# Optimization experiments

Hardware: AMD Instinct MI355X
Metric: run time of the kernel (lower is better)

The kernel has to match this reference:

```python
import jax, jax.numpy as jnp
import numpy as np

B, S1, S2, C = 8, 256, 256, 64
M1, M2 = 32, 32          # n_modes per spatial dim
SCALE = 1.0 / (C * C)    # 1/(in_channels*out_channels)


def setup_inputs() -> dict:
    key = jax.random.key(0)
    ks = jax.random.split(key, 5)
    X = jax.random.normal(ks[0], (B, S1, S2, C), dtype=jnp.float32)
    k0r = SCALE * jax.random.normal(ks[1], (M1, C, C), dtype=jnp.float32)
    k0i = SCALE * jax.random.normal(ks[2], (M1, C, C), dtype=jnp.float32)
    k1r = SCALE * jax.random.normal(ks[3], (M2, C, C), dtype=jnp.float32)
    k1i = SCALE * jax.random.normal(ks[4], (M2, C, C), dtype=jnp.float32)
    return {"X": X, "k0r": k0r, "k0i": k0i, "k1r": k1r, "k1i": k1i}


def reference(X, k0r, k0i, k1r, k1i):
    # Factorized spectral conv: per-spatial-dim rFFT -> truncated-mode
    # complex channel mix -> zero-pad -> irFFT, summed over dims.
    k0 = jax.lax.complex(k0r, k0i)  # (M1, out, in)
    k1 = jax.lax.complex(k1r, k1i)  # (M2, out, in)

    out = jnp.zeros_like(X)

    # --- spatial dim 0 (axis -3) ---
    Xf = jnp.fft.rfft(X, axis=-3, norm="forward")          # (B, S1//2+1, S2, C) complex
    Yt = jnp.einsum("rij,bryj->bryi", k0, Xf[:, :M1])       # truncated-mode channel mix
    Y = jnp.zeros_like(Xf).at[:, :M1].set(Yt)               # zero-pad back to full modes
    out = out + jnp.fft.irfft(Y, n=S1, axis=-3, norm="forward")

    # --- spatial dim 1 (axis -2) ---
    Xf = jnp.fft.rfft(X, axis=-2, norm="forward")           # (B, S1, S2//2+1, C)
    Yt = jnp.einsum("rij,bxrj->bxri", k1, Xf[:, :, :M2])
    Y = jnp.zeros_like(Xf).at[:, :, :M2].set(Yt)
    out = out + jnp.fft.irfft(Y, n=S2, axis=-2, norm="forward")

    return out
```

## Files before the change

### kernel.cpp

```cpp
#include <hip/hip_runtime.h>


namespace {

constexpr int S = 256, C = 64;

typedef _Float16 f16;
typedef _Float16 f16x2 __attribute__((ext_vector_type(2)));
typedef _Float16 f16x4 __attribute__((ext_vector_type(4)));
typedef _Float16 f16x8 __attribute__((ext_vector_type(8)));
typedef float f32x16 __attribute__((ext_vector_type(16)));
typedef unsigned int u32;

constexpr int OFF_FWDF = 0;
constexpr int OFF_INVF = 8192;
constexpr int OFF_A2   = 16384;
constexpr int OFF_PW   = 540672;
constexpr size_t WS_NEED = (size_t)OFF_PW * 4 + (size_t)8 * 256 * 256 * 64 * 2;

constexpr int P   = 4624;
constexpr int LDS_BYTES = 8 * P;

__device__ __host__ inline int cadr(int c) { return c * 16 + (c >> 3) * 16; }
__device__ inline int yadr(int r, int c) { return 1152 * r + c * 4 + (c >> 5) * 16; }

__global__ void k_init_all(const float* __restrict__ k0r, const float* __restrict__ k0i,
                           const float* __restrict__ k1r, const float* __restrict__ ki1,
                           float* __restrict__ ws) {
  const int bid = blockIdx.x;
  if (bid < 128) {
    int t = bid * 256 + threadIdx.x;
    f16* fwdF = (f16*)(ws + OFF_FWDF);
    f16* invF = (f16*)(ws + OFF_INVF);
    if (t < 16384) {
      int e = t & 7, lane = (t >> 3) & 63, mtkk = t >> 9;
      int mt = mtkk & 1, kk = mtkk >> 1;
      int mc = mt * 32 + (lane & 31);
      int x = kk * 16 + 8 * (lane >> 5) + e;
      int r = mc >> 1;
      float ang = (float)((r * x) & 255) * (3.14159265358979323846f / 128.0f);
      float v = (mc & 1) ? -sinf(ang) : cosf(ang);
      fwdF[t] = (f16)v;
    } else {
      int t2 = t - 16384;
      int e = t2 & 7, lane = (t2 >> 3) & 63, mtg = (t2 >> 9) & 7, kk = t2 >> 12;
      int u = mtg * 32 + (lane & 31);
      int mcv = kk * 16 + 8 * (lane >> 5) + e;
      int r = mcv >> 1;
      float wgt = (r == 0) ? 1.0f : 2.0f;
      float ang = (float)((r * u) & 255) * (3.14159265358979323846f / 128.0f);
      float v = (mcv & 1) ? -wgt * sinf(ang) : wgt * cosf(ang);
      invF[t2] = (f16)(v * (1.0f / 256.0f));
    }
    return;
  }
  const int db = bid - 128;
  const float* kr = (db < 2048) ? k0r : k1r;
  const float* ki = (db < 2048) ? k0i : ki1;
  f16* A2 = (f16*)(ws + OFF_A2) + ((db < 2048) ? 0 : 524288);
  int t = (db & 2047) * 256 + threadIdx.x;
  int e = t & 7, l = (t >> 3) & 63, kk = (t >> 9) & 7, mt = (t >> 12) & 3, r = t >> 14;
  int m = mt * 32 + (l & 31);
  int kreal = kk * 16 + 8 * (l >> 5) + e;
  int i = m >> 1, imo = m & 1, j = kreal >> 1, imi = kreal & 1;
  int src = (r * 64 + i) * 64 + j;
  float v = (imi == 0) ? ((imo == 0) ? kr[src] : ki[src])
                       : ((imo == 0) ? -ki[src] : kr[src]);
  A2[t] = (f16)v;
}

template <int MODE>
__launch_bounds__(512, 2)
__global__ void k_dim(const float* __restrict__ X, const float* __restrict__ ws,
                      float* __restrict__ out, f16* __restrict__ pw) {
  constexpr int DIM = (MODE == 0 || MODE == 2) ? 0 : 1;
  __shared__ char sm[LDS_BYTES] __attribute__((aligned(16)));

  const int tid = threadIdx.x;
  const int l = tid & 63, w = tid >> 6;
  const int g2 = l >> 5, l31 = l & 31;
  const int n0 = w * 32;
  const int bid = (DIM == 1) ? (int)(gridDim.x - 1 - blockIdx.x) : (int)blockIdx.x;
  const int b = bid >> 6;
  const int t4 = (bid & 63) * 4;
  const size_t bbase = (size_t)b * (S * S * C);
  const f16* fwdF = (const f16*)(ws + OFF_FWDF);
  const f16* invF = (const f16*)(ws + OFF_INVF);
  const f16* A2 = (const f16*)(ws + OFF_A2) + (DIM == 0 ? 0 : 524288);

  const int colg = n0 + l31;
  const int pp = colg >> 6, jj = colg & 63;

  auto gofs = [&](int u, int c) -> size_t {
    if (DIM == 0)
      return bbase + (size_t)u * (S * C) + (size_t)(t4 + (c >> 6)) * C + (c & 63);
    else
      return bbase + (size_t)(t4 + (c >> 6)) * (S * C) + (size_t)u * C + (c & 63);
  };

  const int ug = w >> 1;
  const int c1 = (w & 1) * 128 + l;
  const int c2 = c1 + 64;

  float r1[8], r2[8];
  auto stage_load = [&](int u0) {
#pragma unroll
    for (int j = 0; j < 8; ++j) r1[j] = X[gofs(u0 + ug * 8 + j, c1)];
#pragma unroll
    for (int j = 0; j < 8; ++j) r2[j] = X[gofs(u0 + ug * 8 + j, c2)];
  };
  auto stage_write = [&](int buf) {
    f16x8 v1, v2;
#pragma unroll
    for (int j = 0; j < 8; ++j) { v1[j] = (f16)r1[j]; v2[j] = (f16)r2[j]; }
    char* base = sm + buf * (4 * P) + ug * P;
    *(f16x8*)(base + cadr(c1)) = v1;
    *(f16x8*)(base + cadr(c2)) = v2;
  };

  f32x16 acc0, acc1;
#pragma unroll
  for (int q = 0; q < 16; ++q) { acc0[q] = 0.f; acc1[q] = 0.f; }

  stage_load(0);
  stage_write(0);
  __syncthreads();

  for (int ch = 0; ch < 8; ++ch) {
    if (ch < 7) stage_load((ch + 1) * 32);
    const char* bbuf = sm + (ch & 1) * (4 * P);
#pragma unroll
    for (int ks = 0; ks < 2; ++ks) {
      const int kk = ch * 2 + ks;
      f16x8 bf = *(const f16x8*)(bbuf + (ks * 2 + g2) * P + cadr(n0 + l31));
      f16x8 a0 = *(const f16x8*)(fwdF + ((size_t)(kk * 2 + 0) * 64 + l) * 8);
      f16x8 a1 = *(const f16x8*)(fwdF + ((size_t)(kk * 2 + 1) * 64 + l) * 8);
      acc0 = __builtin_amdgcn_mfma_f32_32x32x16_f16(a0, bf, acc0, 0, 0, 0);
      acc1 = __builtin_amdgcn_mfma_f32_32x32x16_f16(a1, bf, acc1, 0, 0, 0);
    }
    if (ch < 7) {
      stage_write((ch + 1) & 1);
      __syncthreads();
    }
  }
  __syncthreads();

  {
    const int col = n0 + l31;
    const int p = col >> 6, j = col & 63;
    const int kk = j >> 3, g2p = (j >> 2) & 1, js = j & 3;
#pragma unroll
    for (int pr = 0; pr < 16; ++pr) {
      const int q = (pr & 7) >> 1, hf = pr & 1;
      const int r = 2 * g2 + 4 * q + hf + (pr >> 3) * 16;
      const int reg = 4 * q + 2 * hf;
      const float v0 = (pr < 8) ? acc0[reg] : acc1[reg];
      const float v1 = (pr < 8) ? acc0[reg + 1] : acc1[reg + 1];
      f16x2 v2 = {(f16)v0, (f16)v1};
      const int W = (r * 16 + kk * 2 + g2p) * 4 + p;
      *(f16x2*)(sm + W * 16 + (W >> 3) * 16 + js * 4) = v2;
    }
  }
  __syncthreads();

  {
    const int colsel = l31 & 3;
#pragma unroll 1
    for (int rq = 0; rq < 4; ++rq) {
      const int r = w * 4 + rq;
      f16x8 bfr[8];
#pragma unroll
      for (int kk = 0; kk < 8; ++kk) {
        const int W = (r * 16 + kk * 2 + g2) * 4 + colsel;
        bfr[kk] = *(const f16x8*)(sm + W * 16 + (W >> 3) * 16);
      }
#pragma unroll 1
      for (int mt = 0; mt < 4; ++mt) {
        f32x16 acc;
#pragma unroll
        for (int q = 0; q < 16; ++q) acc[q] = 0.f;
#pragma unroll
        for (int kk = 0; kk < 8; ++kk) {
          f16x8 af = *(const f16x8*)(A2 + ((size_t)((r * 4 + mt) * 8 + kk) * 64 + l) * 8);
          acc = __builtin_amdgcn_mfma_f32_32x32x16_f16(af, bfr[kk], acc, 0, 0, 0);
        }
        if (l31 < 4) {
#pragma unroll
          for (int t2 = 0; t2 < 8; ++t2) {
            int reg = t2 * 2;
            int rowin = (reg & 3) + 8 * (reg >> 2) + 4 * g2;
            int i = (mt * 32 + rowin) >> 1;
            f16x2 v2 = {(f16)acc[reg], (f16)acc[reg + 1]};
            *(f16x2*)(sm + yadr(r, l31 * 64 + i)) = v2;
          }
        }
      }
    }
  }
  __syncthreads();

  f16x8 bf4[4];
  {
    const int cb = colg * 4 + (colg >> 5) * 16;
#pragma unroll
    for (int kk = 0; kk < 4; ++kk) {
      union { f16x8 h; u32 u[4]; } bb;
      const int r0 = 8 * kk + 4 * g2;
#pragma unroll
      for (int s = 0; s < 4; ++s)
        bb.u[s] = *(const u32*)(sm + 1152 * (r0 + s) + cb);
      bf4[kk] = bb.h;
    }
  }

#pragma unroll 1
  for (int h = 0; h < 2; ++h) {
#pragma unroll 1
    for (int mt = 0; mt < 4; ++mt) {
      f32x16 a4;
#pragma unroll
      for (int q = 0; q < 16; ++q) a4[q] = 0.f;

#pragma unroll
      for (int kk = 0; kk < 4; ++kk) {
        f16x8 A = *(const f16x8*)(invF + ((size_t)(kk * 8 + h * 4 + mt) * 64 + l) * 8);
        a4 = __builtin_amdgcn_mfma_f32_32x32x16_f16(A, bf4[kk], a4, 0, 0, 0);
      }

      const int u0 = (h * 4 + mt) * 32;
#pragma unroll
      for (int reg = 0; reg < 16; ++reg) {
        const int u = u0 + (reg & 3) + 8 * (reg >> 2) + 4 * g2;
        if constexpr (MODE == 2) {
          size_t g = bbase + (size_t)u * (S * C) + (size_t)(t4 + pp) * C + jj;
          pw[g] = (f16)a4[reg];
        } else if constexpr (MODE == 3) {
          size_t g = bbase + (size_t)(t4 + pp) * (S * C) + (size_t)u * C + jj;
          out[g] = a4[reg] + (float)pw[g];
        } else {
          size_t g = (DIM == 0)
                         ? bbase + (size_t)u * (S * C) + (size_t)(t4 + pp) * C + jj
                         : bbase + (size_t)(t4 + pp) * (S * C) + (size_t)u * C + jj;
          if constexpr (MODE == 0) out[g] = a4[reg];
          else                     out[g] += a4[reg];
        }
      }
    }
  }
}

}

extern "C" void kernel_launch(void* const* d_in, const int* in_sizes, int n_in,
                              void* d_out, int out_size, void* d_ws, size_t ws_size,
                              hipStream_t stream) {
  (void)in_sizes; (void)n_in; (void)out_size;
  const float* X   = (const float*)d_in[0];
  const float* k0r = (const float*)d_in[1];
  const float* k0i = (const float*)d_in[2];
  const float* k1r = (const float*)d_in[3];
  const float* k1i = (const float*)d_in[4];
  float* out = (float*)d_out;
  float* ws  = (float*)d_ws;
  f16* pw = (f16*)(ws + OFF_PW);

  k_init_all<<<4224, 256, 0, stream>>>(k0r, k0i, k1r, k1i, ws);
  if (ws_size >= WS_NEED) {
    k_dim<2><<<512, 512, 0, stream>>>(X, ws, out, pw);
    k_dim<3><<<512, 512, 0, stream>>>(X, ws, out, pw);
  } else {
    k_dim<0><<<512, 512, 0, stream>>>(X, ws, out, nullptr);
    k_dim<1><<<512, 512, 0, stream>>>(X, ws, out, nullptr);
  }
}
```

Measured before the change: 151.2 us.

## Run dim-1 forward stage concurrently with dim-0 pass via merged kernel

Splits the dim-1 pass: its forward DFT and channel mix run as extra blocks inside a merged launch alongside the full dim-0 pass, writing the mixed spectra to a global scratch buffer. A new lightweight finalize kernel then does the dim-1 inverse DFT and adds the saved dim-0 partial. This doubles the work available in the first launch so both dims' heavy stages can share the GPU, at the cost of an extra global round-trip for the truncated spectra and a larger workspace requirement.

```diff
diff --git a/kernel.cpp b/kernel.cpp
--- a/kernel.cpp
+++ b/kernel.cpp
@@ -16,7 +16,8 @@
 constexpr int OFF_INVF = 8192;
 constexpr int OFF_A2   = 16384;
 constexpr int OFF_PW   = 540672;
-constexpr size_t WS_NEED = (size_t)OFF_PW * 4 + (size_t)8 * 256 * 256 * 64 * 2;
+constexpr int OFF_YT   = 17317888;
+constexpr size_t WS_NEED = (size_t)OFF_YT * 4 + (size_t)512 * 36864;
 
 constexpr int P   = 4624;
 constexpr int LDS_BYTES = 8 * P;
@@ -70,17 +71,15 @@
 }
 
 template <int MODE>
-__launch_bounds__(512, 2)
-__global__ void k_dim(const float* __restrict__ X, const float* __restrict__ ws,
-                      float* __restrict__ out, f16* __restrict__ pw) {
+__device__ void body(int bid, char* sm, const float* __restrict__ X,
+                     const float* __restrict__ ws, float* __restrict__ out,
+                     f16* __restrict__ pw, char* __restrict__ yt) {
   constexpr int DIM = (MODE == 0 || MODE == 2) ? 0 : 1;
-  __shared__ char sm[LDS_BYTES] __attribute__((aligned(16)));
 
   const int tid = threadIdx.x;
   const int l = tid & 63, w = tid >> 6;
   const int g2 = l >> 5, l31 = l & 31;
   const int n0 = w * 32;
-  const int bid = (DIM == 1) ? (int)(gridDim.x - 1 - blockIdx.x) : (int)blockIdx.x;
   const int b = bid >> 6;
   const int t4 = (bid & 63) * 4;
   const size_t bbase = (size_t)b * (S * S * C);
@@ -164,6 +163,7 @@
   __syncthreads();
 
   {
+    char* ytb = (MODE == 4) ? (yt + (size_t)bid * 36864) : sm;
     const int colsel = l31 & 3;
 #pragma unroll 1
     for (int rq = 0; rq < 4; ++rq) {
@@ -191,12 +191,15 @@
             int rowin = (reg & 3) + 8 * (reg >> 2) + 4 * g2;
             int i = (mt * 32 + rowin) >> 1;
             f16x2 v2 = {(f16)acc[reg], (f16)acc[reg + 1]};
-            *(f16x2*)(sm + yadr(r, l31 * 64 + i)) = v2;
+            *(f16x2*)(ytb + yadr(r, l31 * 64 + i)) = v2;
           }
         }
       }
     }
   }
+
+  if constexpr (MODE == 4) return;
+
   __syncthreads();
 
   f16x8 bf4[4];
@@ -234,9 +237,6 @@
         if constexpr (MODE == 2) {
           size_t g = bbase + (size_t)u * (S * C) + (size_t)(t4 + pp) * C + jj;
           pw[g] = (f16)a4[reg];
-        } else if constexpr (MODE == 3) {
-          size_t g = bbase + (size_t)(t4 + pp) * (S * C) + (size_t)u * C + jj;
-          out[g] = a4[reg] + (float)pw[g];
         } else {
           size_t g = (DIM == 0)
                          ? bbase + (size_t)u * (S * C) + (size_t)(t4 + pp) * C + jj
@@ -244,6 +244,79 @@
           if constexpr (MODE == 0) out[g] = a4[reg];
           else                     out[g] += a4[reg];
         }
+      }
+    }
+  }
+}
+
+template <int MODE>
+__launch_bounds__(512, 2)
+__global__ void k_dim(const float* __restrict__ X, const float* __restrict__ ws,
+                      float* __restrict__ out, f16* __restrict__ pw) {
+  __shared__ char sm[LDS_BYTES] __attribute__((aligned(16)));
+  int bid = (MODE == 1) ? (int)(gridDim.x - 1 - blockIdx.x) : (int)blockIdx.x;
+  body<MODE>(bid, sm, X, ws, out, pw, nullptr);
+}
+
+__launch_bounds__(512, 2)
+__global__ void k_merged(const float* __restrict__ X, const float* __restrict__ ws,
+                         float* __restrict__ out, f16* __restrict__ pw,
+                         char* __restrict__ yt) {
+  __shared__ char sm[LDS_BYTES] __attribute__((aligned(16)));
+  if (blockIdx.x < 512) body<2>((int)blockIdx.x, sm, X, ws, out, pw, nullptr);
+  else                  body<4>((int)blockIdx.x - 512, sm, X, ws, out, nullptr, yt);
+}
+
+__launch_bounds__(512, 4)
+__global__ void k_fin(const float* __restrict__ ws, float* __restrict__ out,
+                      const f16* __restrict__ pw, const char* __restrict__ yt) {
+  const int tid = threadIdx.x;
+  const int l = tid & 63, w = tid >> 6;
+  const int g2 = l >> 5, l31 = l & 31;
+  const int n0 = w * 32;
+  const int bid = blockIdx.x;
+  const int b = bid >> 6;
+  const int t4 = (bid & 63) * 4;
+  const size_t bbase = (size_t)b * (S * S * C);
+  const f16* invF = (const f16*)(ws + OFF_INVF);
+  const int colg = n0 + l31;
+  const int pp = colg >> 6, jj = colg & 63;
+  const char* ytb = yt + (size_t)bid * 36864;
+
+  f16x8 bf4[4];
+  {
+    const int cb = colg * 4 + (colg >> 5) * 16;
+#pragma unroll
+    for (int kk = 0; kk < 4; ++kk) {
+      union { f16x8 h; u32 u[4]; } bb;
+      const int r0 = 8 * kk + 4 * g2;
+#pragma unroll
+      for (int s = 0; s < 4; ++s)
+        bb.u[s] = *(const u32*)(ytb + 1152 * (r0 + s) + cb);
+      bf4[kk] = bb.h;
+    }
+  }
+
+#pragma unroll 1
+  for (int h = 0; h < 2; ++h) {
+#pragma unroll 1
+    for (int mt = 0; mt < 4; ++mt) {
+      f32x16 a4;
+#pragma unroll
+      for (int q = 0; q < 16; ++q) a4[q] = 0.f;
+
+#pragma unroll
+      for (int kk = 0; kk < 4; ++kk) {
+        f16x8 A = *(const f16x8*)(invF + ((size_t)(kk * 8 + h * 4 + mt) * 64 + l) * 8);
+        a4 = __builtin_amdgcn_mfma_f32_32x32x16_f16(A, bf4[kk], a4, 0, 0, 0);
+      }
+
+      const int u0 = (h * 4 + mt) * 32;
+#pragma unroll
+      for (int reg = 0; reg < 16; ++reg) {
+        const int u = u0 + (reg & 3) + 8 * (reg >> 2) + 4 * g2;
+        size_t g = bbase + (size_t)(t4 + pp) * (S * C) + (size_t)u * C + jj;
+        out[g] = a4[reg] + (float)pw[g];
       }
     }
   }
@@ -262,12 +335,13 @@
   const float* k1i = (const float*)d_in[4];
   float* out = (float*)d_out;
   float* ws  = (float*)d_ws;
-  f16* pw = (f16*)(ws + OFF_PW);
+  f16* pw  = (f16*)(ws + OFF_PW);
+  char* yt = (char*)(ws + OFF_YT);
 
   k_init_all<<<4224, 256, 0, stream>>>(k0r, k0i, k1r, k1i, ws);
   if (ws_size >= WS_NEED) {
-    k_dim<2><<<512, 512, 0, stream>>>(X, ws, out, pw);
-    k_dim<3><<<512, 512, 0, stream>>>(X, ws, out, pw);
+    k_merged<<<1024, 512, 0, stream>>>(X, ws, out, pw, yt);
+    k_fin<<<512, 512, 0, stream>>>(ws, out, pw, yt);
   } else {
     k_dim<0><<<512, 512, 0, stream>>>(X, ws, out, nullptr);
     k_dim<1><<<512, 512, 0, stream>>>(X, ws, out, nullptr);
```

New measurement: 207.0 us. +36.9%, slower.
